# Performance work log

Hardware: AMD Instinct MI355X
Metric: run time of the kernel (lower is better)

Reference implementation:

```python
import jax, jax.numpy as jnp
import numpy as np

# ---- constants derived from module config ----
DEG_HIST = np.array([0., 12000., 20000., 13000., 4000., 1000.])
AVG_DEG_LOG = float((np.log(np.arange(len(DEG_HIST)) + 1.0) * DEG_HIST).sum() / DEG_HIST.sum())
N_NODES, N_EDGES, N_GRAPHS = 50000, 150000, 2000
D, E_D, TOWERS, F_OUT, N_LAYERS = 75, 50, 5, 15, 4
EPS = 1e-5


def setup_inputs() -> dict:
    key = jax.random.key(0)
    ks = jax.random.split(key, 16)
    g = lambda k, shape, s=0.05: (jax.random.normal(k, shape, jnp.float32) * s)
    return {
        'x': jax.random.randint(ks[0], (N_NODES,), 0, 21),
        'edge_index': jax.random.randint(ks[1], (2, N_EDGES), 0, N_NODES),
        'edge_attr': jax.random.randint(ks[2], (N_EDGES,), 0, 4),
        'batch': jnp.sort(jax.random.randint(ks[3], (N_NODES,), 0, N_GRAPHS)),
        'node_emb': g(ks[4], (21, D), 1.0),
        'edge_emb': g(ks[5], (4, E_D), 1.0),
        'We': g(ks[6], (N_LAYERS, E_D, D)),
        'be': jnp.zeros((N_LAYERS, D), jnp.float32),
        'Wpre': g(ks[7], (N_LAYERS, TOWERS, 3 * D, D)),
        'bpre': jnp.zeros((N_LAYERS, TOWERS, D), jnp.float32),
        'Wpost': g(ks[8], (N_LAYERS, TOWERS, 13 * D, F_OUT)),
        'bpost': jnp.zeros((N_LAYERS, TOWERS, F_OUT), jnp.float32),
        'Wlin': g(ks[9], (N_LAYERS, D, D)),
        'blin': jnp.zeros((N_LAYERS, D), jnp.float32),
        'gamma': jnp.ones((N_LAYERS, D), jnp.float32),
        'beta': jnp.zeros((N_LAYERS, D), jnp.float32),
        'W1': g(ks[10], (D, 50)), 'b1': jnp.zeros((50,), jnp.float32),
        'W2': g(ks[11], (50, 25)), 'b2': jnp.zeros((25,), jnp.float32),
        'W3': g(ks[12], (25, 1)), 'b3': jnp.zeros((1,), jnp.float32),
    }


def _pna_layer(x, src, dst, e_emb, We, be, Wpre, bpre, Wpost, bpost, Wlin, blin):
    # edge encoder (shared across towers)
    e = e_emb @ We + be                                        # [E, D]
    h = jnp.concatenate([x[dst], x[src], e], axis=-1)          # [E, 3D] = (x_i, x_j, e)
    m = jnp.einsum('ec,tcf->etf', h, Wpre) + bpre              # [E, T, D] per-tower pre_nn
    # multi-aggregator scatter (mean / min / max / std) onto target nodes
    deg = jax.ops.segment_sum(jnp.ones((src.shape[0],), x.dtype), dst, num_segments=N_NODES)
    denom = jnp.maximum(deg, 1.0)[:, None, None]
    mean = jax.ops.segment_sum(m, dst, num_segments=N_NODES) / denom
    mean_sq = jax.ops.segment_sum(m * m, dst, num_segments=N_NODES) / denom
    std = jnp.sqrt(jax.nn.relu(mean_sq - mean * mean) + 1e-5)
    has = (deg > 0)[:, None, None]
    mn = jnp.where(has, jax.ops.segment_min(m, dst, num_segments=N_NODES), 0.0)
    mx = jnp.where(has, jax.ops.segment_max(m, dst, num_segments=N_NODES), 0.0)
    agg = jnp.concatenate([mean, mn, mx, std], axis=-1)        # [N, T, 4D]
    # degree scalers: identity / amplification / attenuation
    amp = jnp.log(jnp.maximum(deg, 1.0) + 1.0)[:, None, None] / AVG_DEG_LOG
    out = jnp.concatenate([agg, agg * amp, agg / amp], axis=-1)  # [N, T, 12D]
    xt = jnp.broadcast_to(x[:, None, :], (x.shape[0], TOWERS, D))  # divide_input=False
    out = jnp.concatenate([xt, out], axis=-1)                   # [N, T, 13D]
    out = jnp.einsum('ntc,tcf->ntf', out, Wpost) + bpost        # [N, T, F_OUT] per-tower post_nn
    out = out.reshape(x.shape[0], TOWERS * F_OUT)               # [N, D]
    return out @ Wlin + blin


def _bn(x, gamma, beta):
    mu = x.mean(0)
    var = ((x - mu) ** 2).mean(0)  # biased, training-mode batch stats
    return gamma * (x - mu) / jnp.sqrt(var + EPS) + beta


def reference(x, edge_index, edge_attr, batch, node_emb, edge_emb, We, be, Wpre, bpre,
              Wpost, bpost, Wlin, blin, gamma, beta, W1, b1, W2, b2, W3, b3):
    src, dst = edge_index[0], edge_index[1]
    h = node_emb[x]                 # [N, 75]
    ea = edge_emb[edge_attr]        # [E, 50]
    for l in range(N_LAYERS):
        h = jax.nn.relu(_bn(_pna_layer(h, src, dst, ea, We[l], be[l], Wpre[l], bpre[l],
                                       Wpost[l], bpost[l], Wlin[l], blin[l]),
                            gamma[l], beta[l]))
    pooled = jax.ops.segment_sum(h, batch, num_segments=N_GRAPHS)  # global_add_pool
    z = jax.nn.relu(pooled @ W1 + b1)
    z = jax.nn.relu(z @ W2 + b2)
    return z @ W3 + b3  # [N_GRAPHS, 1]
```

## Files before the change

### kernel.cpp

```cpp
#include <hip/hip_runtime.h>
#include <math.h>

#define NN 50000
#define NE 150000
#define NG 2000
#define NL 4
#define AVG_DEG_LOG 1.1308269950720915f

typedef __attribute__((ext_vector_type(8))) short bf8_t;
typedef __attribute__((ext_vector_type(4))) float f4_t;

__device__ inline unsigned short f2bf(float x) {
  union { float f; unsigned int u; } v; v.f = x;
  unsigned int r = (v.u + 0x7FFFu + ((v.u >> 16) & 1u)) >> 16;
  return (unsigned short)r;
}
__device__ inline float bflo(unsigned int u) { union { unsigned int u; float f; } v; v.u = u << 16; return v.f; }
__device__ inline float bfhi(unsigned int u) { union { unsigned int u; float f; } v; v.u = u & 0xFFFF0000u; return v.f; }

__device__ inline bf8_t ldfrag(const float* __restrict__ zrow, int k0, int bn,
                               const float* __restrict__ musig,
                               const float* __restrict__ gm, const float* __restrict__ bt) {
  bf8_t r;
  #pragma unroll
  for (int j = 0; j < 8; ++j) {
    int k = k0 + j;
    float x = 0.0f;
    if (k < 75) {
      x = zrow[k];
      if (bn) x = fmaxf(gm[k] * (x - musig[k]) * musig[75 + k] + bt[k], 0.0f);
    }
    r[j] = (short)f2bf(x);
  }
  return r;
}

__global__ void k_deg(const int* __restrict__ dst, int* __restrict__ deg) {
  int e = blockIdx.x * 256 + threadIdx.x;
  if (e < NE) atomicAdd(&deg[dst[e]], 1);
}

__global__ __launch_bounds__(1024) void k_scan(const int* __restrict__ deg, int* __restrict__ off) {
  __shared__ int wsum[16];
  __shared__ int wpre[16];
  __shared__ int carry_s;
  int tid = threadIdx.x, lane = tid & 63, wv = tid >> 6;
  if (tid == 0) carry_s = 0;
  __syncthreads();
  for (int base = 0; base < NN; base += 1024) {
    int i = base + tid;
    int v = (i < NN) ? deg[i] : 0;
    int incl = v;
    #pragma unroll
    for (int d = 1; d < 64; d <<= 1) { int t = __shfl_up(incl, d); if (lane >= d) incl += t; }
    if (lane == 63) wsum[wv] = incl;
    __syncthreads();
    if (wv == 0) {
      int s = (lane < 16) ? wsum[lane] : 0;
      int sc = s;
      #pragma unroll
      for (int d = 1; d < 16; d <<= 1) { int t = __shfl_up(sc, d); if (lane >= d) sc += t; }
      if (lane < 16) wpre[lane] = sc - s;
    }
    __syncthreads();
    int carry = carry_s;
    int excl = carry + wpre[wv] + incl - v;
    if (i < NN) off[i] = excl;
    __syncthreads();
    if (tid == 1023) carry_s = excl + v;
    __syncthreads();
  }
  if (tid == 0) off[NN] = carry_s;
}

__global__ void k_amp(const int* __restrict__ deg, const int* __restrict__ off,
                      float* __restrict__ amp, float* __restrict__ invamp,
                      float* __restrict__ gate, int* __restrict__ cursor) {
  int n = blockIdx.x * 256 + threadIdx.x;
  if (n < NN) {
    int d0 = deg[n];
    int d = d0 < 1 ? 1 : d0;
    float a = logf((float)d + 1.0f) / AVG_DEG_LOG;
    amp[n] = a; invamp[n] = 1.0f / a;
    gate[n] = (d0 > 0) ? 1.0f : 0.0f;
    cursor[n] = off[n];
  }
}

__global__ void k_fill(const int* __restrict__ src, const int* __restrict__ dst,
                       const int* __restrict__ attr, int* __restrict__ cursor,
                       unsigned int* __restrict__ cpack) {
  int e = blockIdx.x * 256 + threadIdx.x;
  if (e < NE) {
    int d = dst[e];
    int p = atomicAdd(&cursor[d], 1);
    cpack[p] = (unsigned int)src[e] | ((unsigned int)attr[e] << 16);
  }
}

__global__ void k_embed(const int* __restrict__ x, const float* __restrict__ emb, float* __restrict__ Zf) {
  int i = blockIdx.x * 256 + threadIdx.x;
  if (i < NN * 76) {
    int n = i / 76, c = i - (i / 76) * 76;
    Zf[i] = (c < 75) ? emb[x[n] * 75 + c] : 0.0f;
  }
}

__global__ void k_wxlin(const float* __restrict__ Wpost, const float* __restrict__ Wlin, float* __restrict__ WXlin) {
  int l = blockIdx.x;
  for (int idx = threadIdx.x; idx < 5625; idx += 256) {
    int k = idx / 75, j = idx - (idx / 75) * 75;
    float s = 0.0f;
    for (int o = 0; o < 75; ++o) {
      int t = o / 15, jj = o - t * 15;
      s += Wpost[((l * 5 + t) * 975 + k) * 15 + jj] * Wlin[l * 5625 + o * 75 + j];
    }
    WXlin[l * 5625 + idx] = s;
  }
}

__global__ void k_zb(const float* __restrict__ bpost, const float* __restrict__ blin,
                     const float* __restrict__ Wlin, float* __restrict__ zb) {
  int l = blockIdx.x, j = threadIdx.x;
  if (j < 75) {
    float s = blin[l * 75 + j];
    for (int o = 0; o < 75; ++o) s += bpost[l * 75 + o] * Wlin[l * 5625 + o * 75 + j];
    zb[l * 75 + j] = s;
  }
}

__global__ void k_wy(const float* __restrict__ Wpre, const float* __restrict__ bpre,
                     const float* __restrict__ Wpost, float* __restrict__ WY, float* __restrict__ bY) {
  __shared__ float wsum[1125];
  int b = blockIdx.x;
  int l = b / 15, rr = b - l * 15, t = rr / 3, s = rr - (rr / 3) * 3;
  int tid = threadIdx.x;
  for (int it = tid; it < 1125; it += 256) {
    int f = it / 15, jj = it - (it / 15) * 15;
    float acc = 0.0f;
    #pragma unroll
    for (int agg = 0; agg < 3; ++agg)
      acc += Wpost[((l * 5 + t) * 975 + 75 + s * 300 + agg * 75 + f) * 15 + jj];
    wsum[f * 15 + jj] = acc;
  }
  __syncthreads();
  for (int it = tid; it < 1140; it += 256) {
    int k = it / 15, jj = it - (it / 15) * 15;
    float acc = 0.0f;
    if (k < 75) {
      for (int f = 0; f < 75; ++f)
        acc += Wpre[((l * 5 + t) * 225 + k) * 75 + f] * wsum[f * 15 + jj];
      WY[((l * 3 + s) * 75 + k) * 75 + t * 15 + jj] = acc;
    } else {
      for (int f = 0; f < 75; ++f)
        acc += bpre[l * 375 + t * 75 + f] * wsum[f * 15 + jj];
      bY[(l * 3 + s) * 75 + t * 15 + jj] = acc;
    }
  }
}

__global__ void k_packAll(const float* __restrict__ Wpre, const float* __restrict__ WXlin,
                          const float* __restrict__ WY, const float* __restrict__ Wlin,
                          unsigned short* __restrict__ B1Ts, unsigned short* __restrict__ WXYT,
                          unsigned short* __restrict__ WlinT) {
  const int S1 = 4 * 400 * 96;
  const int S2 = S1 + 4 * 320 * 96;
  const int S3 = S2 + 4 * 80 * 96;
  int idx = blockIdx.x * 256 + threadIdx.x;
  if (idx < S1) {
    int l = idx / (400 * 96); int rem = idx - l * (400 * 96);
    int c = rem / 96, k = rem - (rem / 96) * 96;
    int t = c / 80, f = c - t * 80;
    float v = 0.0f;
    if (f < 75 && k < 75)
      v = Wpre[((l * 5 + t) * 225 + 75 + k) * 75 + f];
    B1Ts[idx] = f2bf(v);
  } else if (idx < S2) {
    int m = idx - S1;
    int l = m / (320 * 96); int rem = m - l * (320 * 96);
    int c = rem / 96, k = rem - (rem / 96) * 96;
    float v = 0.0f;
    if (k < 75) {
      if (c < 80) {
        if (c < 75) v = WXlin[l * 5625 + k * 75 + c];
      } else {
        int g = c - 80; int t = g / 48; int r = g - t * 48; int s = r / 16; int jj = r - s * 16;
        if (jj < 15) v = WY[((l * 3 + s) * 75 + k) * 75 + t * 15 + jj];
      }
    }
    WXYT[m] = f2bf(v);
  } else if (idx < S3) {
    int m = idx - S2;
    int l = m / (80 * 96); int rem = m - l * (80 * 96);
    int j = rem / 96, k = rem - (rem / 96) * 96;
    float v = (j < 75 && k < 75) ? Wlin[l * 5625 + k * 75 + j] : 0.0f;
    WlinT[m] = f2bf(v);
  }
}

__global__ void k_packWcomb(const float* __restrict__ Wpost, unsigned short* __restrict__ WcombT) {
  int idx = blockIdx.x * 256 + threadIdx.x;
  if (idx >= 4 * 5 * 48 * 320) return;
  int l = idx / (5 * 48 * 320); int rem = idx - l * (5 * 48 * 320);
  int t = rem / (48 * 320); rem -= t * (48 * 320);
  int j = rem / 320, k = rem - (rem / 320) * 320;
  int f = k >> 2, agg = k & 3;
  float v = 0.0f;
  if (j < 45 && f < 75) {
    int s = j / 15, jj = j - s * 15;
    v = Wpost[((l * 5 + t) * 975 + 75 + s * 300 + agg * 75 + f) * 15 + jj];
  }
  WcombT[idx] = f2bf(v);
}

__global__ void k_etab(const float* __restrict__ edge_emb, const float* __restrict__ We,
                       const float* __restrict__ be, const float* __restrict__ Wpre,
                       float* __restrict__ etab) {
  __shared__ float ev[75];
  int l = blockIdx.x >> 2, a = blockIdx.x & 3;
  int tid = threadIdx.x;
  if (tid < 75) {
    float acc = be[l * 75 + tid];
    for (int k = 0; k < 50; ++k) acc += edge_emb[a * 50 + k] * We[(l * 50 + k) * 75 + tid];
    ev[tid] = acc;
  }
  __syncthreads();
  for (int c = tid; c < 400; c += 256) {
    int t = c / 80, f = c - t * 80;
    float acc = 0.0f;
    if (f < 75) {
      for (int d = 0; d < 75; ++d) acc += ev[d] * Wpre[((l * 5 + t) * 225 + 150 + d) * 75 + f];
    }
    etab[(l * 4 + a) * 400 + c] = acc;
  }
}

__global__ __launch_bounds__(256) void k_gemm1(const float* __restrict__ Zf,
                                               const float* __restrict__ bnsum,
                                               const float* __restrict__ gm, const float* __restrict__ bt,
                                               int bn,
                                               const unsigned short* __restrict__ B1Ts_l,
                                               unsigned short* __restrict__ Hsrc,
                                               unsigned short* __restrict__ hb) {
  __shared__ float ms_s[150];
  __shared__ __align__(16) unsigned short H_s[64 * 408];
  int tid = threadIdx.x;
  if (tid < 75) {
    float mu = bnsum[tid] * (1.0f / NN);
    float var = fmaxf(bnsum[75 + tid] * (1.0f / NN) - mu * mu, 0.0f);
    ms_s[tid] = mu;
    ms_s[75 + tid] = 1.0f / sqrtf(var + 1e-5f);
  }
  __syncthreads();
  int w = tid >> 6, lane = tid & 63;
  int l15 = lane & 15, l4 = lane >> 4;
  int m0 = blockIdx.x * 64;
  int mA = m0 + w * 16 + l15; if (mA >= NN) mA = NN - 1;
  const float* zrow = Zf + (size_t)mA * 76;
  bf8_t a0 = ldfrag(zrow, l4 * 8, bn, ms_s, gm, bt);
  bf8_t a1 = ldfrag(zrow, 32 + l4 * 8, bn, ms_s, gm, bt);
  bf8_t a2 = ldfrag(zrow, 64 + l4 * 8, bn, ms_s, gm, bt);
  {
    unsigned short* hrow = hb + (size_t)mA * 96 + l4 * 8;
    *(bf8_t*)(hrow) = a0;
    *(bf8_t*)(hrow + 32) = a1;
    *(bf8_t*)(hrow + 64) = a2;
  }
  for (int nf = 0; nf < 25; ++nf) {
    int c = nf * 16 + l15;
    const unsigned short* bp = B1Ts_l + (size_t)c * 96 + l4 * 8;
    f4_t acc = {0.f, 0.f, 0.f, 0.f};
    acc = __builtin_amdgcn_mfma_f32_16x16x32_bf16(a0, *(const bf8_t*)(bp), acc, 0, 0, 0);
    acc = __builtin_amdgcn_mfma_f32_16x16x32_bf16(a1, *(const bf8_t*)(bp + 32), acc, 0, 0, 0);
    acc = __builtin_amdgcn_mfma_f32_16x16x32_bf16(a2, *(const bf8_t*)(bp + 64), acc, 0, 0, 0);
    #pragma unroll
    for (int i = 0; i < 4; ++i)
      H_s[(w * 16 + l4 * 4 + i) * 408 + c] = f2bf(acc[i]);
  }
  __syncthreads();
  for (int idx = tid; idx < 3200; idx += 256) {
    int row = idx / 50, q = idx - row * 50;
    int m = m0 + row;
    if (m < NN)
      *(uint4*)&Hsrc[(size_t)m * 400 + q * 8] = *(const uint4*)&H_s[row * 408 + q * 8];
  }
}

__global__ __launch_bounds__(256) void k_gather(const unsigned short* __restrict__ Hsrc,
                                                const int* __restrict__ off,
                                                const unsigned int* __restrict__ cpack,
                                                const float* __restrict__ etab_l,
                                                unsigned short* __restrict__ A) {
  __shared__ float et_s[1600];
  int tid = threadIdx.x, w = tid >> 6, lane = tid & 63;
  for (int it = tid; it < 1600; it += 256) {
    int aa = it / 400, c = it - aa * 400;
    et_s[aa * 400 + (c ^ (((c >> 3) & 7) << 2))] = etab_l[it];
  }
  __syncthreads();
  if (lane >= 50) return;
  int g = blockIdx.x * 4 + w;
  int e0 = off[g], e1 = off[g + 1];
  int c0 = lane * 8;
  int cs = c0 ^ (((c0 >> 3) & 7) << 2);
  int t = lane / 10;
  int f0 = c0 - t * 80;
  const bf8_t* hbase = (const bf8_t*)Hsrc + lane;
  float s8[8], q8[8], mn8[8], mx8[8];
  #pragma unroll
  for (int j = 0; j < 8; ++j) {
    s8[j] = 0.0f; q8[j] = 0.0f;
    mn8[j] = 3.402823466e+38f; mx8[j] = -3.402823466e+38f;
  }
  auto acc8 = [&](bf8_t hv, unsigned int aa) {
    union { bf8_t v; unsigned int u[4]; } cv; cv.v = hv;
    f4_t ea = *(const f4_t*)&et_s[aa * 400 + cs];
    f4_t eb = *(const f4_t*)&et_s[aa * 400 + (cs ^ 4)];
    #pragma unroll
    for (int j = 0; j < 8; ++j) {
      float h = (j & 1) ? bfhi(cv.u[j >> 1]) : bflo(cv.u[j >> 1]);
      float e = (j < 4) ? ea[j] : eb[j - 4];
      float q = h + e;
      s8[j] += q;
      q8[j] = fmaf(q, q, q8[j]);
      mn8[j] = fminf(mn8[j], q);
      mx8[j] = fmaxf(mx8[j], q);
    }
  };
  for (int e = e0; e < e1; ) {
    int m = e1 - e;
    unsigned int pk0 = cpack[e];
    unsigned int pk1 = cpack[m > 1 ? e + 1 : e];
    unsigned int pk2 = cpack[m > 2 ? e + 2 : e];
    unsigned int pk3 = cpack[m > 3 ? e + 3 : e];
    bf8_t h0 = hbase[(pk0 & 0xFFFFu) * 50];
    bf8_t h1 = hbase[(pk1 & 0xFFFFu) * 50];
    bf8_t h2 = hbase[(pk2 & 0xFFFFu) * 50];
    bf8_t h3 = hbase[(pk3 & 0xFFFFu) * 50];
    acc8(h0, pk0 >> 16);
    if (m > 1) acc8(h1, pk1 >> 16);
    if (m > 2) acc8(h2, pk2 >> 16);
    if (m > 3) acc8(h3, pk3 >> 16);
    e += (m < 4) ? m : 4;
  }
  int d = e1 - e0;
  unsigned short* abase = A + ((size_t)t * NN + g) * 320 + f0 * 4;
  uint4 pk[4];
  unsigned int* pw = (unsigned int*)pk;
  if (d > 0) {
    float inv = 1.0f / (float)d;
    #pragma unroll
    for (int j = 0; j < 8; ++j) {
      float mu = s8[j] * inv;
      float sd = sqrtf(fmaxf(q8[j] * inv - mu * mu, 0.0f) + 1e-5f);
      pw[j * 2]     = (unsigned int)f2bf(mu) | ((unsigned int)f2bf(mn8[j]) << 16);
      pw[j * 2 + 1] = (unsigned int)f2bf(mx8[j]) | ((unsigned int)f2bf(sd) << 16);
    }
  } else {
    unsigned int zsd = (unsigned int)f2bf(0.0031622776601683794f) << 16;
    #pragma unroll
    for (int j = 0; j < 8; ++j) { pw[j * 2] = 0u; pw[j * 2 + 1] = zsd; }
  }
  #pragma unroll
  for (int jj = 0; jj < 4; ++jj) *(uint4*)(abase + jj * 8) = pk[jj];
}

__global__ __launch_bounds__(256) void k_ptower(const unsigned short* __restrict__ A,
                                                const unsigned short* __restrict__ hb,
                                                const unsigned short* __restrict__ WcombT_l,
                                                const unsigned short* __restrict__ WXYT_l,
                                                const float* __restrict__ ampv,
                                                const float* __restrict__ invampv,
                                                const float* __restrict__ gatev,
                                                const float* __restrict__ bY_l,
                                                unsigned short* __restrict__ Cbg) {
  __shared__ __align__(16) float Out_s[64 * 99];
  __shared__ float amp_s[64], inv_s[64], gate_s[64];
  __shared__ float bY_s[45];
  int tid = threadIdx.x;
  int w = tid >> 6, lane = tid & 63;
  int l15 = lane & 15, l4 = lane >> 4;
  int t = blockIdx.x;
  int m0 = blockIdx.y * 64;

  for (int r = tid; r < 64; r += 256) {
    int m = m0 + r; if (m >= NN) m = NN - 1;
    amp_s[r] = ampv[m]; inv_s[r] = invampv[m]; gate_s[r] = gatev[m];
  }
  if (tid < 45) {
    int s = tid / 15, jj = tid - s * 15;
    bY_s[tid] = bY_l[s * 75 + t * 15 + jj];
  }
  int mh = m0 + w * 16 + l15; if (mh >= NN) mh = NN - 1;
  const unsigned short* arow = A + ((size_t)t * NN + mh) * 320 + l4 * 8;
  bf8_t af[10];
  #pragma unroll
  for (int ks = 0; ks < 10; ++ks) af[ks] = *(const bf8_t*)(arow + ks * 32);
  const unsigned short* hrow = hb + (size_t)mh * 96 + l4 * 8;
  bf8_t hb0 = *(const bf8_t*)(hrow);
  bf8_t hb1 = *(const bf8_t*)(hrow + 32);
  bf8_t hb2 = *(const bf8_t*)(hrow + 64);

  f4_t tw0 = {0.f,0.f,0.f,0.f}, tw1 = {0.f,0.f,0.f,0.f}, tw2 = {0.f,0.f,0.f,0.f};
  const unsigned short* wp0 = WcombT_l + (size_t)(t * 48 + l15) * 320 + l4 * 8;
  const unsigned short* wp1 = WcombT_l + (size_t)(t * 48 + 16 + l15) * 320 + l4 * 8;
  const unsigned short* wp2 = WcombT_l + (size_t)(t * 48 + 32 + l15) * 320 + l4 * 8;
  #pragma unroll
  for (int ks = 0; ks < 10; ++ks) {
    tw0 = __builtin_amdgcn_mfma_f32_16x16x32_bf16(af[ks], *(const bf8_t*)(wp0 + ks * 32), tw0, 0, 0, 0);
    tw1 = __builtin_amdgcn_mfma_f32_16x16x32_bf16(af[ks], *(const bf8_t*)(wp1 + ks * 32), tw1, 0, 0, 0);
    tw2 = __builtin_amdgcn_mfma_f32_16x16x32_bf16(af[ks], *(const bf8_t*)(wp2 + ks * 32), tw2, 0, 0, 0);
  }
  f4_t yv[3];
  #pragma unroll
  for (int s = 0; s < 3; ++s) {
    const unsigned short* bp = WXYT_l + (size_t)(80 + t * 48 + s * 16 + l15) * 96 + l4 * 8;
    f4_t acc = {0.f, 0.f, 0.f, 0.f};
    acc = __builtin_amdgcn_mfma_f32_16x16x32_bf16(hb0, *(const bf8_t*)(bp), acc, 0, 0, 0);
    acc = __builtin_amdgcn_mfma_f32_16x16x32_bf16(hb1, *(const bf8_t*)(bp + 32), acc, 0, 0, 0);
    acc = __builtin_amdgcn_mfma_f32_16x16x32_bf16(hb2, *(const bf8_t*)(bp + 64), acc, 0, 0, 0);
    yv[s] = acc;
  }
  #pragma unroll
  for (int i = 0; i < 4; ++i) {
    int rb = w * 16 + l4 * 4 + i;
    Out_s[rb * 99 + l15] = tw0[i];
    Out_s[rb * 99 + 16 + l15] = tw1[i];
    Out_s[rb * 99 + 32 + l15] = tw2[i];
    Out_s[rb * 99 + 48 + l15] = yv[0][i];
    Out_s[rb * 99 + 64 + l15] = yv[1][i];
    Out_s[rb * 99 + 80 + l15] = yv[2][i];
  }
  __syncthreads();
  for (int item = tid; item < 1024; item += 256) {
    int r = item >> 4, jj = item & 15;
    int m = m0 + r;
    if (jj < 15 && m < NN) {
      const float* ob = &Out_s[r * 99];
      float gt = gate_s[r];
      float v1 = ob[jj]      + gt * (ob[48 + jj] + bY_s[jj]);
      float v2 = ob[15 + jj] + gt * (ob[64 + jj] + bY_s[15 + jj]);
      float v3 = ob[30 + jj] + gt * (ob[80 + jj] + bY_s[30 + jj]);
      Cbg[(size_t)m * 96 + t * 15 + jj] = f2bf(v1 + amp_s[r] * v2 + inv_s[r] * v3);
    }
  }
}

__global__ __launch_bounds__(256) void k_lin(const unsigned short* __restrict__ Cbg,
                                             const unsigned short* __restrict__ hb,
                                             const unsigned short* __restrict__ WXYT_l,
                                             const unsigned short* __restrict__ WlinT_l,
                                             const float* __restrict__ zb_l,
                                             float* __restrict__ Zf,
                                             float* __restrict__ bnsum) {
  __shared__ float bnred[152];
  int tid = threadIdx.x;
  int w = tid >> 6, lane = tid & 63;
  int l15 = lane & 15, l4 = lane >> 4;
  int m0 = blockIdx.x * 64;
  if (tid < 152) bnred[tid] = 0.0f;
  __syncthreads();
  int mh = m0 + w * 16 + l15; if (mh >= NN) mh = NN - 1;
  const unsigned short* hrow = hb + (size_t)mh * 96 + l4 * 8;
  bf8_t hb0 = *(const bf8_t*)(hrow);
  bf8_t hb1 = *(const bf8_t*)(hrow + 32);
  bf8_t hb2 = *(const bf8_t*)(hrow + 64);
  const unsigned short* crow = Cbg + (size_t)mh * 96 + l4 * 8;
  bf8_t cf0 = *(const bf8_t*)(crow);
  bf8_t cf1 = *(const bf8_t*)(crow + 32);
  bf8_t cf2 = *(const bf8_t*)(crow + 64);
  #pragma unroll
  for (int fx = 0; fx < 5; ++fx) {
    int cc = fx * 16 + l15;
    const unsigned short* xp = WXYT_l + (size_t)cc * 96 + l4 * 8;
    f4_t x0 = {0.f, 0.f, 0.f, 0.f};
    x0 = __builtin_amdgcn_mfma_f32_16x16x32_bf16(hb0, *(const bf8_t*)(xp), x0, 0, 0, 0);
    x0 = __builtin_amdgcn_mfma_f32_16x16x32_bf16(hb1, *(const bf8_t*)(xp + 32), x0, 0, 0, 0);
    x0 = __builtin_amdgcn_mfma_f32_16x16x32_bf16(hb2, *(const bf8_t*)(xp + 64), x0, 0, 0, 0);
    const unsigned short* bp = WlinT_l + (size_t)cc * 96 + l4 * 8;
    f4_t acc = {0.f, 0.f, 0.f, 0.f};
    acc = __builtin_amdgcn_mfma_f32_16x16x32_bf16(cf0, *(const bf8_t*)(bp), acc, 0, 0, 0);
    acc = __builtin_amdgcn_mfma_f32_16x16x32_bf16(cf1, *(const bf8_t*)(bp + 32), acc, 0, 0, 0);
    acc = __builtin_amdgcn_mfma_f32_16x16x32_bf16(cf2, *(const bf8_t*)(bp + 64), acc, 0, 0, 0);
    if (cc < 75) {
      float s = 0.0f, q = 0.0f;
      #pragma unroll
      for (int i = 0; i < 4; ++i) {
        int m = m0 + w * 16 + l4 * 4 + i;
        if (m < NN) {
          float z = acc[i] + x0[i] + zb_l[cc];
          Zf[(size_t)m * 76 + cc] = z;
          s += z; q = fmaf(z, z, q);
        }
      }
      s += __shfl_xor(s, 16); q += __shfl_xor(q, 16);
      s += __shfl_xor(s, 32); q += __shfl_xor(q, 32);
      if (l4 == 0) {
        atomicAdd(&bnred[cc], s);
        atomicAdd(&bnred[76 + cc], q);
      }
    }
  }
  __syncthreads();
  if (tid < 75) atomicAdd(&bnsum[tid], bnred[tid]);
  else if (tid >= 76 && tid < 151) atomicAdd(&bnsum[tid - 1], bnred[tid]);
}

__global__ __launch_bounds__(128) void k_pool_mlp(const float* __restrict__ Zf, const int* __restrict__ batch,
                                                  const float* __restrict__ bnsum,
                                                  const float* __restrict__ gm, const float* __restrict__ bt,
                                                  const float* __restrict__ W1, const float* __restrict__ b1,
                                                  const float* __restrict__ W2, const float* __restrict__ b2,
                                                  const float* __restrict__ W3, const float* __restrict__ b3,
                                                  float* __restrict__ out) {
  __shared__ float pooled[75];
  __shared__ float ms_s[150];
  __shared__ float z1[50];
  __shared__ float z2[25];
  __shared__ int se[2];
  int g = blockIdx.x, tid = threadIdx.x;
  if (tid < 2) {
    int target = g + tid;
    int lo = 0, hi = NN;
    while (lo < hi) { int mid = (lo + hi) >> 1; if (batch[mid] < target) lo = mid + 1; else hi = mid; }
    se[tid] = lo;
  }
  if (tid < 75) {
    float mu = bnsum[tid] * (1.0f / NN);
    float var = fmaxf(bnsum[75 + tid] * (1.0f / NN) - mu * mu, 0.0f);
    ms_s[tid] = mu;
    ms_s[75 + tid] = 1.0f / sqrtf(var + 1e-5f);
  }
  __syncthreads();
  int s = se[0], e = se[1];
  if (tid < 75) {
    float mu = ms_s[tid], sig = ms_s[75 + tid], gmc = gm[tid], btc = bt[tid];
    float acc = 0.0f;
    for (int r = s; r < e; ++r)
      acc += fmaxf(gmc * (Zf[(size_t)r * 76 + tid] - mu) * sig + btc, 0.0f);
    pooled[tid] = acc;
  }
  __syncthreads();
  if (tid < 50) {
    float acc = b1[tid];
    for (int c = 0; c < 75; ++c) acc += pooled[c] * W1[c * 50 + tid];
    z1[tid] = fmaxf(acc, 0.0f);
  }
  __syncthreads();
  if (tid < 25) {
    float acc = b2[tid];
    for (int c = 0; c < 50; ++c) acc += z1[c] * W2[c * 25 + tid];
    z2[tid] = fmaxf(acc, 0.0f);
  }
  __syncthreads();
  if (tid == 0) {
    float acc = b3[0];
    for (int c = 0; c < 25; ++c) acc += z2[c] * W3[c];
    out[g] = acc;
  }
}

extern "C" void kernel_launch(void* const* d_in, const int* in_sizes, int n_in,
                              void* d_out, int out_size, void* d_ws, size_t ws_size,
                              hipStream_t stream) {
  const int* x = (const int*)d_in[0];
  const int* ei = (const int*)d_in[1];
  const int* eattr = (const int*)d_in[2];
  const int* batch = (const int*)d_in[3];
  const float* node_emb = (const float*)d_in[4];
  const float* edge_emb = (const float*)d_in[5];
  const float* We = (const float*)d_in[6];
  const float* be = (const float*)d_in[7];
  const float* Wpre = (const float*)d_in[8];
  const float* bpre = (const float*)d_in[9];
  const float* Wpost = (const float*)d_in[10];
  const float* bpost = (const float*)d_in[11];
  const float* Wlin = (const float*)d_in[12];
  const float* blin = (const float*)d_in[13];
  const float* gamma = (const float*)d_in[14];
  const float* beta = (const float*)d_in[15];
  const float* W1 = (const float*)d_in[16];
  const float* b1 = (const float*)d_in[17];
  const float* W2 = (const float*)d_in[18];
  const float* b2 = (const float*)d_in[19];
  const float* W3 = (const float*)d_in[20];
  const float* b3 = (const float*)d_in[21];
  float* out = (float*)d_out;

  const int* src = ei;
  const int* dst = ei + NE;

  char* p = (char*)d_ws;
  auto alloc = [&](size_t bytes) { char* r = p; p += (bytes + 255) & ~(size_t)255; return r; };
  int* deg     = (int*)alloc((size_t)NN * 4);
  int* off     = (int*)alloc((size_t)(NN + 1) * 4);
  int* cursor  = (int*)alloc((size_t)NN * 4);
  unsigned int* cpack = (unsigned int*)alloc((size_t)NE * 4);
  float* amp    = (float*)alloc((size_t)NN * 4);
  float* invamp = (float*)alloc((size_t)NN * 4);
  float* gate   = (float*)alloc((size_t)NN * 4);
  float* Zf            = (float*)alloc((size_t)NN * 76 * 4 + 256);
  unsigned short* Hsrc = (unsigned short*)alloc((size_t)NN * 400 * 2 + 256);
  unsigned short* hbv  = (unsigned short*)alloc((size_t)NN * 96 * 2 + 256);
  unsigned short* Cbg  = (unsigned short*)alloc((size_t)NN * 96 * 2 + 256);
  unsigned short* Abuf = (unsigned short*)alloc((size_t)5 * NN * 320 * 2 + 256);
  unsigned short* B1Ts   = (unsigned short*)alloc((size_t)4 * 400 * 96 * 2);
  unsigned short* WXYT   = (unsigned short*)alloc((size_t)4 * 320 * 96 * 2);
  unsigned short* WlinT  = (unsigned short*)alloc((size_t)4 * 80 * 96 * 2);
  unsigned short* WcombT = (unsigned short*)alloc((size_t)4 * 5 * 48 * 320 * 2);
  float* WXlin = (float*)alloc((size_t)4 * 5625 * 4);
  float* WY    = (float*)alloc((size_t)4 * 3 * 75 * 75 * 4);
  float* bY    = (float*)alloc((size_t)4 * 3 * 75 * 4);
  float* zb    = (float*)alloc((size_t)4 * 75 * 4);
  float* etab  = (float*)alloc((size_t)4 * 4 * 400 * 4);
  float* bnsum  = (float*)alloc((size_t)4 * 152 * 4);

  hipMemsetAsync(deg, 0, (size_t)NN * 4, stream);
  hipMemsetAsync(bnsum, 0, (size_t)4 * 152 * 4, stream);
  k_deg<<<(NE + 255) / 256, 256, 0, stream>>>(dst, deg);
  k_scan<<<1, 1024, 0, stream>>>(deg, off);
  k_amp<<<(NN + 255) / 256, 256, 0, stream>>>(deg, off, amp, invamp, gate, cursor);
  k_fill<<<(NE + 255) / 256, 256, 0, stream>>>(src, dst, eattr, cursor, cpack);
  k_embed<<<(NN * 76 + 255) / 256, 256, 0, stream>>>(x, node_emb, Zf);
  k_wxlin<<<4, 256, 0, stream>>>(Wpost, Wlin, WXlin);
  k_wy<<<60, 256, 0, stream>>>(Wpre, bpre, Wpost, WY, bY);
  k_zb<<<4, 128, 0, stream>>>(bpost, blin, Wlin, zb);
  {
    int tot = 4 * 400 * 96 + 4 * 320 * 96 + 4 * 80 * 96;
    k_packAll<<<(tot + 255) / 256, 256, 0, stream>>>(Wpre, WXlin, WY, Wlin, B1Ts, WXYT, WlinT);
  }
  k_packWcomb<<<(4 * 5 * 48 * 320 + 255) / 256, 256, 0, stream>>>(Wpost, WcombT);
  k_etab<<<16, 256, 0, stream>>>(edge_emb, We, be, Wpre, etab);

  for (int l = 0; l < NL; ++l) {
    const float* gm = gamma + (l > 0 ? (l - 1) * 75 : 0);
    const float* bt = beta + (l > 0 ? (l - 1) * 75 : 0);
    int bn = (l > 0) ? 1 : 0;
    const float* bnsum_prev = bnsum + (size_t)(l > 0 ? l - 1 : 0) * 152;
    float* bnsum_cur = bnsum + (size_t)l * 152;
    k_gemm1<<<(NN + 63) / 64, 256, 0, stream>>>(Zf, bnsum_prev, gm, bt, bn,
                                                B1Ts + (size_t)l * 400 * 96, Hsrc, hbv);
    k_gather<<<NN / 4, 256, 0, stream>>>(Hsrc, off, cpack, etab + (size_t)l * 4 * 400, Abuf);
    {
      dim3 gp(5, (NN + 63) / 64);
      k_ptower<<<gp, 256, 0, stream>>>(Abuf, hbv,
                                       WcombT + (size_t)l * 5 * 48 * 320,
                                       WXYT + (size_t)l * 320 * 96,
                                       amp, invamp, gate,
                                       bY + (size_t)l * 225, Cbg);
    }
    k_lin<<<(NN + 63) / 64, 256, 0, stream>>>(Cbg, hbv,
                                              WXYT + (size_t)l * 320 * 96,
                                              WlinT + (size_t)l * 80 * 96,
                                              zb + l * 75, Zf, bnsum_cur);
  }
  k_pool_mlp<<<NG, 128, 0, stream>>>(Zf, batch, bnsum + (size_t)(NL - 1) * 152,
                                     gamma + 225, beta + 225,
                                     W1, b1, W2, b2, W3, b3, out);
}
```

Before: 1.200 ms.

## Parallelize degree scan and weight-precompute kernels across many blocks

Replaces the single-block serial prefix scan over node degrees with a three-pass multi-block scan: per-block scan, a scan of the block sums, then a per-element add. It also spreads the k_wxlin and k_wy weight-folding kernels over a 2D grid so each thread computes one output instead of looping within a few blocks. This targets setup kernels that used only a handful of CUs. The cost is two extra kernel launches, and k_wy now recomputes its shared wsum tile in every y-block.

```diff
diff --git a/kernel.cpp b/kernel.cpp
--- a/kernel.cpp
+++ b/kernel.cpp
@@ -40,37 +40,44 @@
   if (e < NE) atomicAdd(&deg[dst[e]], 1);
 }
 
-__global__ __launch_bounds__(1024) void k_scan(const int* __restrict__ deg, int* __restrict__ off) {
+__global__ __launch_bounds__(1024) void k_scan1(const int* __restrict__ deg, int* __restrict__ off,
+                                                int* __restrict__ bsum) {
   __shared__ int wsum[16];
   __shared__ int wpre[16];
-  __shared__ int carry_s;
   int tid = threadIdx.x, lane = tid & 63, wv = tid >> 6;
-  if (tid == 0) carry_s = 0;
-  __syncthreads();
-  for (int base = 0; base < NN; base += 1024) {
-    int i = base + tid;
-    int v = (i < NN) ? deg[i] : 0;
-    int incl = v;
+  int i = blockIdx.x * 1024 + tid;
+  int v = (i < NN) ? deg[i] : 0;
+  int incl = v;
+  #pragma unroll
+  for (int d = 1; d < 64; d <<= 1) { int t = __shfl_up(incl, d); if (lane >= d) incl += t; }
+  if (lane == 63) wsum[wv] = incl;
+  __syncthreads();
+  if (wv == 0) {
+    int s = (lane < 16) ? wsum[lane] : 0;
+    int sc = s;
     #pragma unroll
-    for (int d = 1; d < 64; d <<= 1) { int t = __shfl_up(incl, d); if (lane >= d) incl += t; }
-    if (lane == 63) wsum[wv] = incl;
-    __syncthreads();
-    if (wv == 0) {
-      int s = (lane < 16) ? wsum[lane] : 0;
-      int sc = s;
-      #pragma unroll
-      for (int d = 1; d < 16; d <<= 1) { int t = __shfl_up(sc, d); if (lane >= d) sc += t; }
-      if (lane < 16) wpre[lane] = sc - s;
-    }
-    __syncthreads();
-    int carry = carry_s;
-    int excl = carry + wpre[wv] + incl - v;
-    if (i < NN) off[i] = excl;
-    __syncthreads();
-    if (tid == 1023) carry_s = excl + v;
-    __syncthreads();
-  }
-  if (tid == 0) off[NN] = carry_s;
+    for (int d = 1; d < 16; d <<= 1) { int t = __shfl_up(sc, d); if (lane >= d) sc += t; }
+    if (lane < 16) wpre[lane] = sc - s;
+  }
+  __syncthreads();
+  int excl = wpre[wv] + incl - v;
+  if (i < NN) off[i] = excl;
+  if (tid == 1023) bsum[blockIdx.x] = excl + v;
+}
+
+__global__ void k_scan2(const int* __restrict__ bsum, int* __restrict__ bpre, int* __restrict__ off) {
+  int lane = threadIdx.x;
+  int v = (lane < 49) ? bsum[lane] : 0;
+  int incl = v;
+  #pragma unroll
+  for (int d = 1; d < 64; d <<= 1) { int t = __shfl_up(incl, d); if (lane >= d) incl += t; }
+  if (lane < 49) bpre[lane] = incl - v;
+  if (lane == 63) off[NN] = incl;
+}
+
+__global__ void k_scan3(const int* __restrict__ bpre, int* __restrict__ off) {
+  int i = blockIdx.x * 256 + threadIdx.x;
+  if (i < NN) off[i] += bpre[i >> 10];
 }
 
 __global__ void k_amp(const int* __restrict__ deg, const int* __restrict__ off,
@@ -108,7 +115,8 @@
 
 __global__ void k_wxlin(const float* __restrict__ Wpost, const float* __restrict__ Wlin, float* __restrict__ WXlin) {
   int l = blockIdx.x;
-  for (int idx = threadIdx.x; idx < 5625; idx += 256) {
+  int idx = blockIdx.y * 256 + threadIdx.x;
+  if (idx < 5625) {
     int k = idx / 75, j = idx - (idx / 75) * 75;
     float s = 0.0f;
     for (int o = 0; o < 75; ++o) {
@@ -144,7 +152,9 @@
     wsum[f * 15 + jj] = acc;
   }
   __syncthreads();
-  for (int it = tid; it < 1140; it += 256) {
+  int it0 = blockIdx.y * 228;
+  int it1 = it0 + 228;
+  for (int it = it0 + tid; it < it1; it += 256) {
     int k = it / 15, jj = it - (it / 15) * 15;
     float acc = 0.0f;
     if (k < 75) {
@@ -595,6 +605,8 @@
   int* deg     = (int*)alloc((size_t)NN * 4);
   int* off     = (int*)alloc((size_t)(NN + 1) * 4);
   int* cursor  = (int*)alloc((size_t)NN * 4);
+  int* bsum    = (int*)alloc((size_t)64 * 4);
+  int* bpre2   = (int*)alloc((size_t)64 * 4);
   unsigned int* cpack = (unsigned int*)alloc((size_t)NE * 4);
   float* amp    = (float*)alloc((size_t)NN * 4);
   float* invamp = (float*)alloc((size_t)NN * 4);
@@ -618,12 +630,14 @@
   hipMemsetAsync(deg, 0, (size_t)NN * 4, stream);
   hipMemsetAsync(bnsum, 0, (size_t)4 * 152 * 4, stream);
   k_deg<<<(NE + 255) / 256, 256, 0, stream>>>(dst, deg);
-  k_scan<<<1, 1024, 0, stream>>>(deg, off);
+  k_scan1<<<(NN + 1023) / 1024, 1024, 0, stream>>>(deg, off, bsum);
+  k_scan2<<<1, 64, 0, stream>>>(bsum, bpre2, off);
+  k_scan3<<<(NN + 255) / 256, 256, 0, stream>>>(bpre2, off);
   k_amp<<<(NN + 255) / 256, 256, 0, stream>>>(deg, off, amp, invamp, gate, cursor);
   k_fill<<<(NE + 255) / 256, 256, 0, stream>>>(src, dst, eattr, cursor, cpack);
   k_embed<<<(NN * 76 + 255) / 256, 256, 0, stream>>>(x, node_emb, Zf);
-  k_wxlin<<<4, 256, 0, stream>>>(Wpost, Wlin, WXlin);
-  k_wy<<<60, 256, 0, stream>>>(Wpre, bpre, Wpost, WY, bY);
+  k_wxlin<<<dim3(4, 23), 256, 0, stream>>>(Wpost, Wlin, WXlin);
+  k_wy<<<dim3(60, 5), 256, 0, stream>>>(Wpre, bpre, Wpost, WY, bY);
   k_zb<<<4, 128, 0, stream>>>(bpost, blin, Wlin, zb);
   {
     int tot = 4 * 400 * 96 + 4 * 320 * 96 + 4 * 80 * 96;
```

After: 1.072 ms. 1.12x faster.
